# Kernel tuning notes

Hardware: AMD Instinct MI355X
Metric: run time of the kernel (lower is better)

The kernel has to match this reference:

```python
import jax, jax.numpy as jnp
import numpy as np

EPS_ANGLE = 1e-8   # eps in _cos_angle's F.normalize
EPS_NORM = 1e-12   # default F.normalize eps used for the similarity matrix
TOPK = 4
EXTRA_FRAMES = (1, 3, 5, 7)          # teacher-only frames
SHARED_TEACHER = (2, 4, 6)           # shared frames in teacher indexing
SHARED_STUDENT = (1, 2, 3)           # same frames in student indexing
W1 = W2 = W3 = 1.0


def _angle_cosines(ref, shared, sim):
    """Cosines of the 3 RKD angles for every (ref r, shared s, sim k) triplet.
    ref: [B,R,D], shared: [B,S,D], sim: [B,R,K,D]. Returns 3 arrays [B,R,S,K].
    Uses the dot-product expansion (u-v).(w-v) = uw - uv - vw + vv so the
    [B,R,S,K,D] difference tensors are never materialized (same math as the
    chunked torch loop)."""
    rr = jnp.sum(ref * ref, -1)                       # [B,R]
    ss = jnp.sum(shared * shared, -1)                 # [B,S]
    hh = jnp.sum(sim * sim, -1)                       # [B,R,K]
    sr = jnp.einsum('brd,bsd->brs', ref, shared)      # [B,R,S]
    rh = jnp.einsum('brd,brkd->brk', ref, sim)        # [B,R,K]
    sh = jnp.einsum('bsd,brkd->brsk', shared, sim)    # [B,R,S,K]
    rr_ = rr[:, :, None, None]
    ss_ = ss[:, None, :, None]
    hh_ = hh[:, :, None, :]
    sr_ = sr[..., None]
    rh_ = rh[:, :, None, :]
    n_sr = jnp.sqrt(jnp.maximum(ss_ - 2 * sr_ + rr_, 0.0))  # ||shared-ref||
    n_hr = jnp.sqrt(jnp.maximum(hh_ - 2 * rh_ + rr_, 0.0))  # ||sim-ref||
    n_sh = jnp.sqrt(jnp.maximum(ss_ - 2 * sh + hh_, 0.0))   # ||shared-sim||
    cl = lambda n: jnp.maximum(n, EPS_ANGLE)
    a1 = (sh - rh_ - sr_ + rr_) / (cl(n_sr) * cl(n_hr))  # angle at ref
    a2 = (sr_ - sh - rh_ + hh_) / (cl(n_hr) * cl(n_sh))  # angle at sim
    a3 = (rh_ - sr_ - sh + ss_) / (cl(n_sr) * cl(n_sh))  # angle at shared
    return a1, a2, a3


def _l2n(x, eps):
    return x / jnp.maximum(jnp.linalg.norm(x, axis=-1, keepdims=True), eps)


def setup_inputs() -> dict:
    key = jax.random.key(0)
    k1, k2, k3, k4 = jax.random.split(key, 4)
    B, P, D = 4, 1024, 1024
    return {
        'teacher_feats': jax.random.normal(k1, (B, 8, P, D), dtype=jnp.float32),
        'student_feats': jax.random.normal(k2, (B, 4, P, D), dtype=jnp.float32),
        'ref_perm': jax.random.randint(k3, (256,), 0, P),
        'shared_perm': jax.random.randint(k4, (256,), 0, P),
    }


def reference(teacher_feats, student_feats, ref_perm, shared_perm):
    B, St, P, D = teacher_feats.shape
    R = ref_perm.shape[0]
    S = shared_perm.shape[0]
    sg = jax.lax.stop_gradient

    ref_t = sg(teacher_feats[:, 0, ref_perm, :])        # [B,R,D]
    ref_s = student_feats[:, 0, ref_perm, :]            # [B,R,D]

    # teacher-only (extra) frames, concatenated along patch dim -> [B,4P,D]
    extra_t = sg(teacher_feats[:, jnp.array(EXTRA_FRAMES), :, :]).reshape(B, len(EXTRA_FRAMES) * P, D)
    sim = jnp.einsum('brd,bed->bre', _l2n(ref_t, EPS_NORM), _l2n(extra_t, EPS_NORM))
    _, topk_idx = jax.lax.top_k(sim, TOPK)              # [B,R,K]
    sim_high = jax.vmap(lambda e, i: e[i])(extra_t, topk_idx)  # [B,R,K,D]
    sim_high = sg(sim_high)

    s1 = s2 = s3 = jnp.float32(0.0)
    for ti, si in zip(SHARED_TEACHER, SHARED_STUDENT):
        sh_t = sg(teacher_feats[:, ti, shared_perm, :])
        sh_s = student_feats[:, si, shared_perm, :]
        a1t, a2t, a3t = _angle_cosines(ref_t, sh_t, sim_high)
        a1s, a2s, a3s = _angle_cosines(ref_s, sh_s, sim_high)
        s1 = s1 + jnp.sum(jnp.abs(a1s - sg(a1t)))
        s2 = s2 + jnp.sum(jnp.abs(a2s - sg(a2t)))
        s3 = s3 + jnp.sum(jnp.abs(a3s - sg(a3t)))

    total_elements = len(SHARED_TEACHER) * B * R * S * TOPK
    loss = (W1 * s1 + W2 * s2 + W3 * s3) / total_elements
    return loss
```

## Files before the change

kernel.cpp:

```cpp
#include <hip/hip_runtime.h>
#include <float.h>

#define BB 4
#define PP 1024
#define DD 1024
#define RR 256
#define SSZ 256
#define KT 4
#define EE 4096
#define NPAIR 3

typedef float  f32x4  __attribute__((ext_vector_type(4)));
typedef short  short8 __attribute__((ext_vector_type(8)));

#define MFMA16(a,b,c) __builtin_amdgcn_mfma_f32_16x16x32_bf16((a),(b),(c),0,0,0)

#define OFF_NE    ((size_t)0)
#define OFF_RR_T  ((size_t)16384)
#define OFF_RR_S  ((size_t)17408)
#define OFF_HH    ((size_t)18432)
#define OFF_RH_T  ((size_t)22528)
#define OFF_RH_S  ((size_t)26624)
#define OFF_SS_T  ((size_t)30720)
#define OFF_SS_S  ((size_t)33792)
#define OFF_TOPK  ((size_t)36864)
#define OFF_ACC   ((size_t)40960)
#define OFF_CAND  ((size_t)45056)
#define FLOAT_END ((size_t)569344)

#define U_REF_T ((size_t)0)
#define U_REF_S ((size_t)2097152)
#define U_SIMH  ((size_t)4194304)
#define U_SH_T  ((size_t)8388608)
#define U_SH_S  ((size_t)11534336)
#define U_EXT   ((size_t)14680064)

__device__ inline float block_sum256(float v, float* sb) {
  v += __shfl_down(v, 32); v += __shfl_down(v, 16);
  v += __shfl_down(v, 8);  v += __shfl_down(v, 4);
  v += __shfl_down(v, 2);  v += __shfl_down(v, 1);
  int lane = threadIdx.x & 63, wid = threadIdx.x >> 6;
  if (lane == 0) sb[wid] = v;
  __syncthreads();
  float r = 0.f;
  if (threadIdx.x < 4) r = sb[threadIdx.x];
  r += __shfl_down(r, 2); r += __shfl_down(r, 1);
  __syncthreads();
  return r;
}

__device__ inline float dot4(const float4& a, const float4& b) {
  return a.x*b.x + a.y*b.y + a.z*b.z + a.w*b.w;
}

__device__ inline unsigned short bhi(float x) {
  unsigned u = __float_as_uint(x);
  return (unsigned short)((u + 0x7fffu + ((u >> 16) & 1u)) >> 16);
}
__device__ inline ushort4 h4of(float4 f) {
  return make_ushort4(bhi(f.x), bhi(f.y), bhi(f.z), bhi(f.w));
}

__device__ inline size_t wofs(size_t base, int R, int t) {
  int rr = R & 15;
  int ss = ((t >> 1) & 3) ^ ((rr >> 1) & 3);
  return base + (size_t)(R >> 4)*16384 + (size_t)(t >> 3)*512
       + rr*32 + ss*8 + (t & 1)*4;
}

__global__ __launch_bounds__(256) void k_prep(const float* __restrict__ T,
                                              const float* __restrict__ Sf,
                                              const int* __restrict__ ref_perm,
                                              const int* __restrict__ shared_perm,
                                              float* __restrict__ ws) {
  __shared__ float sb[4];
  ushort* uws = (ushort*)(ws + FLOAT_END);
  int blk = blockIdx.x;
  int t = threadIdx.x;
  if (blk < 1024) {
    int b = blk >> 8, r = blk & 255;
    int pos = ref_perm[r];
    const float4* ts = (const float4*)(T  + ((size_t)(b*8 + 0)*PP + pos)*DD);
    const float4* sv = (const float4*)(Sf + ((size_t)(b*4 + 0)*PP + pos)*DD);
    float4 a = ts[t], c = sv[t];
    int R = b*RR + r;
    *(ushort4*)(uws + wofs(U_REF_T, R, t)) = h4of(a);
    *(ushort4*)(uws + wofs(U_REF_S, R, t)) = h4of(c);
    float r1 = block_sum256(dot4(a, a), sb);
    float r2 = block_sum256(dot4(c, c), sb);
    if (t == 0) {
      ws[OFF_RR_T + R] = r1;
      ws[OFF_RR_S + R] = r2;
    }
  } else if (blk < 17408) {
    int i = blk - 1024;
    int b = i >> 12, e = i & 4095;
    int f = 1 + 2*(e >> 10);
    int pos = e & 1023;
    const float4* src = (const float4*)(T + ((size_t)(b*8 + f)*PP + pos)*DD);
    float4 a = src[t];
    *(ushort4*)(uws + wofs(U_EXT, b*EE + e, t)) = h4of(a);
    float tot = block_sum256(dot4(a, a), sb);
    if (t == 0) ws[OFF_NE + (size_t)b*EE + e] = fmaxf(sqrtf(tot), 1e-12f);
  } else {
    int idx = blk - 17408;
    int p = idx / (BB*SSZ);
    int b = (idx / SSZ) % BB;
    int s = idx % SSZ;
    int pos = shared_perm[s];
    int ti = 2*(p + 1), si = p + 1;
    const float4* tr = (const float4*)(T  + ((size_t)(b*8 + ti)*PP + pos)*DD);
    const float4* sr = (const float4*)(Sf + ((size_t)(b*4 + si)*PP + pos)*DD);
    float4 a = tr[t], c = sr[t];
    *(ushort4*)(uws + wofs(U_SH_T, idx, t)) = h4of(a);
    *(ushort4*)(uws + wofs(U_SH_S, idx, t)) = h4of(c);
    float r1 = block_sum256(dot4(a, a), sb);
    float r2 = block_sum256(dot4(c, c), sb);
    if (t == 0) { ws[OFF_SS_T + idx] = r1; ws[OFF_SS_S + idx] = r2; }
  }
}

__global__ __launch_bounds__(256) void k_sim(float* __restrict__ ws) {
  __shared__ float simv[4][16][68];
  const ushort* uws = (const ushort*)(ws + FLOAT_END);
  int d = blockIdx.x;
  int u8 = d & 7, q = d >> 3;
  int b = u8 >> 1, eh = u8 & 1;
  int eb = eh*32 + (q >> 2);
  int rgq = q & 3;
  int tid = threadIdx.x;
  int w = tid >> 6, lane = tid & 63;
  int rg = rgq*4 + w;
  int r0 = rg*16, e0 = eb*64;
  int l15 = lane & 15, lq = (lane >> 4) & 3;
  int laneoff = l15*32 + ((lq ^ ((l15 >> 1) & 3)))*8;

  const ushort* pA = uws + U_REF_T + ((size_t)((b*RR + r0) >> 4))*16384 + laneoff;
  const ushort* pB0 = uws + U_EXT + ((size_t)((b*EE + e0) >> 4) + 0)*16384 + laneoff;
  const ushort* pB1 = uws + U_EXT + ((size_t)((b*EE + e0) >> 4) + 1)*16384 + laneoff;
  const ushort* pB2 = uws + U_EXT + ((size_t)((b*EE + e0) >> 4) + 2)*16384 + laneoff;
  const ushort* pB3 = uws + U_EXT + ((size_t)((b*EE + e0) >> 4) + 3)*16384 + laneoff;

  f32x4 acc[4];
#pragma unroll
  for (int j = 0; j < 4; ++j) acc[j] = (f32x4){0.f, 0.f, 0.f, 0.f};

#pragma unroll 4
  for (int c = 0; c < 32; ++c) {
    int o = c*512;
    short8 ah = *(const short8*)(pA + o);
    short8 b0 = *(const short8*)(pB0 + o);
    short8 b1 = *(const short8*)(pB1 + o);
    short8 b2 = *(const short8*)(pB2 + o);
    short8 b3 = *(const short8*)(pB3 + o);
    acc[0] = MFMA16(ah, b0, acc[0]);
    acc[1] = MFMA16(ah, b1, acc[1]);
    acc[2] = MFMA16(ah, b2, acc[2]);
    acc[3] = MFMA16(ah, b3, acc[3]);
  }

  float invs[4];
#pragma unroll
  for (int j = 0; j < 4; ++j)
    invs[j] = 1.f / ws[OFF_NE + (size_t)b*EE + e0 + j*16 + l15];
#pragma unroll
  for (int j = 0; j < 4; ++j)
#pragma unroll
    for (int q2 = 0; q2 < 4; ++q2)
      simv[w][lq*4 + q2][j*16 + l15] = acc[j][q2] * invs[j];
  if (lane < 16) {
    float v[4] = {-FLT_MAX, -FLT_MAX, -FLT_MAX, -FLT_MAX};
    int ix[4] = {0x7fffffff, 0x7fffffff, 0x7fffffff, 0x7fffffff};
#pragma unroll 1
    for (int e = 0; e < 64; ++e) {
      float f = simv[w][lane][e];
      if (f > v[3]) {
        int eg = e0 + e;
        if (f > v[0])      { v[3]=v[2]; ix[3]=ix[2]; v[2]=v[1]; ix[2]=ix[1]; v[1]=v[0]; ix[1]=ix[0]; v[0]=f; ix[0]=eg; }
        else if (f > v[1]) { v[3]=v[2]; ix[3]=ix[2]; v[2]=v[1]; ix[2]=ix[1]; v[1]=f; ix[1]=eg; }
        else if (f > v[2]) { v[3]=v[2]; ix[3]=ix[2]; v[2]=f; ix[2]=eg; }
        else               { v[3]=f; ix[3]=eg; }
      }
    }
    float2* cand = (float2*)(ws + OFF_CAND);
    size_t base = (((size_t)(b*RR + r0 + lane))*64 + eb)*4;
#pragma unroll
    for (int k = 0; k < 4; ++k)
      cand[base + k] = make_float2(v[k], __int_as_float(ix[k]));
  }
}

__global__ __launch_bounds__(256) void k_select(const float* __restrict__ T,
                                                const float* __restrict__ Sf,
                                                const int* __restrict__ ref_perm,
                                                float* __restrict__ ws) {
  __shared__ float rv[256];
  __shared__ int   ri[256];
  __shared__ int   winIdx;
  __shared__ int   sel[4];
  int br = blockIdx.x;
  int tid = threadIdx.x;
  const float2* cand = (const float2*)(ws + OFF_CAND);
  float2 c0 = cand[(size_t)br*256 + tid];
  float v = c0.x;
  int idx = __float_as_int(c0.y);
  int* outi = (int*)(ws + OFF_TOPK) + (size_t)br*KT;
  for (int k = 0; k < KT; ++k) {
    rv[tid] = v; ri[tid] = idx;
    __syncthreads();
    for (int off = 128; off > 0; off >>= 1) {
      if (tid < off) {
        float v2 = rv[tid+off]; int i2 = ri[tid+off];
        if (v2 > rv[tid] || (v2 == rv[tid] && i2 < ri[tid])) { rv[tid] = v2; ri[tid] = i2; }
      }
      __syncthreads();
    }
    if (tid == 0) { outi[k] = ri[0]; winIdx = ri[0]; sel[k] = ri[0]; }
    __syncthreads();
    if (idx == winIdx) v = -FLT_MAX;
    __syncthreads();
  }

  int b = br >> 8, r = br & 255;
  int g = tid >> 6, lane = tid & 63;
  int e = sel[g];
  int rpos = ref_perm[r];
  const float4* src = (const float4*)(T + ((size_t)(b*8 + 1 + 2*(e >> 10))*PP + (e & 1023))*DD);
  const float4* rt  = (const float4*)(T  + ((size_t)(b*8 + 0)*PP + rpos)*DD);
  const float4* rs  = (const float4*)(Sf + ((size_t)(b*4 + 0)*PP + rpos)*DD);
  ushort* uws = (ushort*)(ws + FLOAT_END);
  int rowi = br*KT + g;
  float hh = 0.f, rht = 0.f, rhs = 0.f;
#pragma unroll
  for (int i = 0; i < 4; ++i) {
    int t4 = lane*4 + i;
    float4 h = src[t4];
    *(ushort4*)(uws + wofs(U_SIMH, rowi, t4)) = h4of(h);
    float4 a = rt[t4], c = rs[t4];
    hh  += dot4(h, h);
    rht += dot4(h, a);
    rhs += dot4(h, c);
  }
  hh  += __shfl_down(hh, 32);  hh  += __shfl_down(hh, 16);
  hh  += __shfl_down(hh, 8);   hh  += __shfl_down(hh, 4);
  hh  += __shfl_down(hh, 2);   hh  += __shfl_down(hh, 1);
  rht += __shfl_down(rht, 32); rht += __shfl_down(rht, 16);
  rht += __shfl_down(rht, 8);  rht += __shfl_down(rht, 4);
  rht += __shfl_down(rht, 2);  rht += __shfl_down(rht, 1);
  rhs += __shfl_down(rhs, 32); rhs += __shfl_down(rhs, 16);
  rhs += __shfl_down(rhs, 8);  rhs += __shfl_down(rhs, 4);
  rhs += __shfl_down(rhs, 2);  rhs += __shfl_down(rhs, 1);
  if (lane == 0) {
    ws[OFF_HH + rowi]   = hh;
    ws[OFF_RH_T + rowi] = rht;
    ws[OFF_RH_S + rowi] = rhs;
  }
}

__global__ __launch_bounds__(192) void k_main(float* __restrict__ ws,
                                              double* __restrict__ acc_out) {
  __shared__ float Ct[3][80][17];
  __shared__ float Cs2[3][80][17];
  __shared__ float sb[3];
  const ushort* uws = (const ushort*)(ws + FLOAT_END);

  int d = blockIdx.x;
  int u8 = d & 7, q = d >> 3;
  int b = u8 >> 1, rhalf = u8 & 1;
  int tid = threadIdx.x;
  int w = tid >> 6, lane = tid & 63;
  int t = q*3 + w;
  int p = t >> 6;
  int rem = t & 63;
  int s32i = rem >> 3, r16q = rem & 7;
  int z = p*4 + b;
  int r16i = rhalf*8 + r16q;
  int r0 = r16i*16, s0 = s32i*32;

  int l15 = lane & 15, lq = (lane >> 4) & 3;
  int laneoff = l15*32 + ((lq ^ ((l15 >> 1) & 3)))*8;

  const ushort* pa0; const ushort* pa1; const ushort* pa2; const ushort* pa3;
  const ushort* prt; const ushort* prs;
  const ushort* pbt0; const ushort* pbt1; const ushort* pbs0; const ushort* pbs1;
  {
    size_t gs = (size_t)((b*RR + r0) >> 2);
    pa0 = uws + U_SIMH + (gs + 0)*16384 + laneoff;
    pa1 = uws + U_SIMH + (gs + 1)*16384 + laneoff;
    pa2 = uws + U_SIMH + (gs + 2)*16384 + laneoff;
    pa3 = uws + U_SIMH + (gs + 3)*16384 + laneoff;
    size_t gr = (size_t)((b*RR + r0) >> 4);
    prt = uws + U_REF_T + gr*16384 + laneoff;
    prs = uws + U_REF_S + gr*16384 + laneoff;
    size_t gh = (size_t)((z*SSZ + s0) >> 4);
    pbt0 = uws + U_SH_T + (gh + 0)*16384 + laneoff;
    pbt1 = uws + U_SH_T + (gh + 1)*16384 + laneoff;
    pbs0 = uws + U_SH_S + (gh + 0)*16384 + laneoff;
    pbs1 = uws + U_SH_S + (gh + 1)*16384 + laneoff;
  }

  f32x4 aT0[2], aT1[2], aT2[2], aT3[2], aRT[2];
  f32x4 aS0[2], aS1[2], aS2[2], aS3[2], aRS[2];
#pragma unroll
  for (int h = 0; h < 2; ++h) {
    aT0[h] = aT1[h] = aT2[h] = aT3[h] = aRT[h] = (f32x4){0.f,0.f,0.f,0.f};
    aS0[h] = aS1[h] = aS2[h] = aS3[h] = aRS[h] = (f32x4){0.f,0.f,0.f,0.f};
  }

#pragma unroll 2
  for (int c = 0; c < 32; ++c) {
    int o = c*512;
    short8 bt0 = *(const short8*)(pbt0 + o);
    short8 bt1 = *(const short8*)(pbt1 + o);
    short8 bs0 = *(const short8*)(pbs0 + o);
    short8 bs1 = *(const short8*)(pbs1 + o);
    short8 a0 = *(const short8*)(pa0 + o);
    short8 a1 = *(const short8*)(pa1 + o);
    short8 a2 = *(const short8*)(pa2 + o);
    short8 a3 = *(const short8*)(pa3 + o);
    short8 rt = *(const short8*)(prt + o);
    short8 rs = *(const short8*)(prs + o);
    aT0[0] = MFMA16(a0, bt0, aT0[0]);  aT0[1] = MFMA16(a0, bt1, aT0[1]);
    aT1[0] = MFMA16(a1, bt0, aT1[0]);  aT1[1] = MFMA16(a1, bt1, aT1[1]);
    aT2[0] = MFMA16(a2, bt0, aT2[0]);  aT2[1] = MFMA16(a2, bt1, aT2[1]);
    aT3[0] = MFMA16(a3, bt0, aT3[0]);  aT3[1] = MFMA16(a3, bt1, aT3[1]);
    aRT[0] = MFMA16(rt, bt0, aRT[0]);  aRT[1] = MFMA16(rt, bt1, aRT[1]);
    aS0[0] = MFMA16(a0, bs0, aS0[0]);  aS0[1] = MFMA16(a0, bs1, aS0[1]);
    aS1[0] = MFMA16(a1, bs0, aS1[0]);  aS1[1] = MFMA16(a1, bs1, aS1[1]);
    aS2[0] = MFMA16(a2, bs0, aS2[0]);  aS2[1] = MFMA16(a2, bs1, aS2[1]);
    aS3[0] = MFMA16(a3, bs0, aS3[0]);  aS3[1] = MFMA16(a3, bs1, aS3[1]);
    aRS[0] = MFMA16(rs, bs0, aRS[0]);  aRS[1] = MFMA16(rs, bs1, aRS[1]);
  }

  int rl = lane >> 2, sg = lane & 3;
  int r = r0 + rl;
  float rrt = ws[OFF_RR_T + b*RR + r];
  float rrs = ws[OFF_RR_S + b*RR + r];
  float hhk[4], rhtk[4], rhsk[4], ihr_t[4], ihr_s[4];
#pragma unroll
  for (int k = 0; k < 4; ++k) {
    int idx = (b*RR + r)*KT + k;
    hhk[k]  = ws[OFF_HH + idx];
    rhtk[k] = ws[OFF_RH_T + idx];
    rhsk[k] = ws[OFF_RH_S + idx];
    float nt = sqrtf(fmaxf(hhk[k] - 2.f*rhtk[k] + rrt, 0.f));
    float ns = sqrtf(fmaxf(hhk[k] - 2.f*rhsk[k] + rrs, 0.f));
    ihr_t[k] = 1.f / fmaxf(nt, 1e-8f);
    ihr_s[k] = 1.f / fmaxf(ns, 1e-8f);
  }

  float local = 0.f;
#pragma unroll
  for (int h = 0; h < 2; ++h) {
#pragma unroll
    for (int q2 = 0; q2 < 4; ++q2) {
      int rg = lq*4 + q2;
      Ct[w][ 0 + rg][l15] = aT0[h][q2];
      Ct[w][16 + rg][l15] = aT1[h][q2];
      Ct[w][32 + rg][l15] = aT2[h][q2];
      Ct[w][48 + rg][l15] = aT3[h][q2];
      Ct[w][64 + rg][l15] = aRT[h][q2];
      Cs2[w][ 0 + rg][l15] = aS0[h][q2];
      Cs2[w][16 + rg][l15] = aS1[h][q2];
      Cs2[w][32 + rg][l15] = aS2[h][q2];
      Cs2[w][48 + rg][l15] = aS3[h][q2];
      Cs2[w][64 + rg][l15] = aRS[h][q2];
    }
#pragma unroll
    for (int j = 0; j < 4; ++j) {
      int sl = sg*4 + j;
      int sidx = z*SSZ + s0 + h*16 + sl;
      float sst = ws[OFF_SS_T + sidx];
      float sss = ws[OFF_SS_S + sidx];
      float srt = Ct[w][64 + rl][sl];
      float srs = Cs2[w][64 + rl][sl];
      float isr_t = 1.f / fmaxf(sqrtf(fmaxf(sst - 2.f*srt + rrt, 0.f)), 1e-8f);
      float isr_s = 1.f / fmaxf(sqrtf(fmaxf(sss - 2.f*srs + rrs, 0.f)), 1e-8f);
#pragma unroll
      for (int k = 0; k < 4; ++k) {
        float sht = Ct[w][rl*4 + k][sl];
        float shs = Cs2[w][rl*4 + k][sl];
        float ish_t = 1.f / fmaxf(sqrtf(fmaxf(sst - 2.f*sht + hhk[k], 0.f)), 1e-8f);
        float ish_s = 1.f / fmaxf(sqrtf(fmaxf(sss - 2.f*shs + hhk[k], 0.f)), 1e-8f);
        float a1t = (sht - rhtk[k] - srt + rrt) * (isr_t * ihr_t[k]);
        float a2t = (srt - sht - rhtk[k] + hhk[k]) * (ihr_t[k] * ish_t);
        float a3t = (rhtk[k] - srt - sht + sst) * (isr_t * ish_t);
        float a1s = (shs - rhsk[k] - srs + rrs) * (isr_s * ihr_s[k]);
        float a2s = (srs - shs - rhsk[k] + hhk[k]) * (ihr_s[k] * ish_s);
        float a3s = (rhsk[k] - srs - shs + sss) * (isr_s * ish_s);
        local += fabsf(a1s - a1t) + fabsf(a2s - a2t) + fabsf(a3s - a3t);
      }
    }
  }

  float v = local;
  v += __shfl_down(v, 32); v += __shfl_down(v, 16);
  v += __shfl_down(v, 8);  v += __shfl_down(v, 4);
  v += __shfl_down(v, 2);  v += __shfl_down(v, 1);
  if (lane == 0) sb[w] = v;
  __syncthreads();
  if (tid == 0) atomicAdd(acc_out, (double)(sb[0] + sb[1] + sb[2]));
}

__global__ void k_final(const double* __restrict__ acc, float* __restrict__ out) {
  out[0] = (float)(acc[0] / 3145728.0);
}

extern "C" void kernel_launch(void* const* d_in, const int* in_sizes, int n_in,
                              void* d_out, int out_size, void* d_ws, size_t ws_size,
                              hipStream_t stream) {
  const float* T  = (const float*)d_in[0];
  const float* Sf = (const float*)d_in[1];
  const int* ref_perm    = (const int*)d_in[2];
  const int* shared_perm = (const int*)d_in[3];
  float* ws = (float*)d_ws;
  double* acc = (double*)(ws + OFF_ACC);

  hipMemsetAsync(acc, 0, sizeof(double), stream);
  k_prep<<<20480, 256, 0, stream>>>(T, Sf, ref_perm, shared_perm, ws);
  k_sim<<<1024, 256, 0, stream>>>(ws);
  k_select<<<BB*RR, 256, 0, stream>>>(T, Sf, ref_perm, ws);
  k_main<<<512, 192, 0, stream>>>(ws, acc);
  k_final<<<1, 1, 0, stream>>>(acc, (float*)d_out);
}
```

Measured before the change: 118.1 us.

## Widen k_main shared tile to 64 columns and fuse final division via last-block counter

Measured after the change: 140.5 us. 1.19x slower.

```diff
diff --git a/kernel.cpp b/kernel.cpp
--- a/kernel.cpp
+++ b/kernel.cpp
@@ -258,7 +258,8 @@
 }
 
 __global__ __launch_bounds__(192) void k_main(float* __restrict__ ws,
-                                              double* __restrict__ acc_out) {
+                                              double* __restrict__ acc_out,
+                                              float* __restrict__ out) {
   __shared__ float Ct[3][80][17];
   __shared__ float Cs2[3][80][17];
   __shared__ float sb[3];
@@ -270,19 +271,19 @@
   int tid = threadIdx.x;
   int w = tid >> 6, lane = tid & 63;
   int t = q*3 + w;
-  int p = t >> 6;
-  int rem = t & 63;
-  int s32i = rem >> 3, r16q = rem & 7;
+  int p = t >> 5;
+  int rem = t & 31;
+  int s64i = rem >> 3, r16q = rem & 7;
   int z = p*4 + b;
   int r16i = rhalf*8 + r16q;
-  int r0 = r16i*16, s0 = s32i*32;
+  int r0 = r16i*16, s0 = s64i*64;
 
   int l15 = lane & 15, lq = (lane >> 4) & 3;
   int laneoff = l15*32 + ((lq ^ ((l15 >> 1) & 3)))*8;
 
   const ushort* pa0; const ushort* pa1; const ushort* pa2; const ushort* pa3;
   const ushort* prt; const ushort* prs;
-  const ushort* pbt0; const ushort* pbt1; const ushort* pbs0; const ushort* pbs1;
+  const ushort* pbt[4]; const ushort* pbs[4];
   {
     size_t gs = (size_t)((b*RR + r0) >> 2);
     pa0 = uws + U_SIMH + (gs + 0)*16384 + laneoff;
@@ -293,43 +294,45 @@
     prt = uws + U_REF_T + gr*16384 + laneoff;
     prs = uws + U_REF_S + gr*16384 + laneoff;
     size_t gh = (size_t)((z*SSZ + s0) >> 4);
-    pbt0 = uws + U_SH_T + (gh + 0)*16384 + laneoff;
-    pbt1 = uws + U_SH_T + (gh + 1)*16384 + laneoff;
-    pbs0 = uws + U_SH_S + (gh + 0)*16384 + laneoff;
-    pbs1 = uws + U_SH_S + (gh + 1)*16384 + laneoff;
-  }
-
-  f32x4 aT0[2], aT1[2], aT2[2], aT3[2], aRT[2];
-  f32x4 aS0[2], aS1[2], aS2[2], aS3[2], aRS[2];
-#pragma unroll
-  for (int h = 0; h < 2; ++h) {
+#pragma unroll
+    for (int j = 0; j < 4; ++j) {
+      pbt[j] = uws + U_SH_T + (gh + j)*16384 + laneoff;
+      pbs[j] = uws + U_SH_S + (gh + j)*16384 + laneoff;
+    }
+  }
+
+  f32x4 aT0[4], aT1[4], aT2[4], aT3[4], aRT[4];
+  f32x4 aS0[4], aS1[4], aS2[4], aS3[4], aRS[4];
+#pragma unroll
+  for (int h = 0; h < 4; ++h) {
     aT0[h] = aT1[h] = aT2[h] = aT3[h] = aRT[h] = (f32x4){0.f,0.f,0.f,0.f};
     aS0[h] = aS1[h] = aS2[h] = aS3[h] = aRS[h] = (f32x4){0.f,0.f,0.f,0.f};
   }
 
-#pragma unroll 2
+#pragma unroll 1
   for (int c = 0; c < 32; ++c) {
     int o = c*512;
-    short8 bt0 = *(const short8*)(pbt0 + o);
-    short8 bt1 = *(const short8*)(pbt1 + o);
-    short8 bs0 = *(const short8*)(pbs0 + o);
-    short8 bs1 = *(const short8*)(pbs1 + o);
     short8 a0 = *(const short8*)(pa0 + o);
     short8 a1 = *(const short8*)(pa1 + o);
     short8 a2 = *(const short8*)(pa2 + o);
     short8 a3 = *(const short8*)(pa3 + o);
     short8 rt = *(const short8*)(prt + o);
     short8 rs = *(const short8*)(prs + o);
-    aT0[0] = MFMA16(a0, bt0, aT0[0]);  aT0[1] = MFMA16(a0, bt1, aT0[1]);
-    aT1[0] = MFMA16(a1, bt0, aT1[0]);  aT1[1] = MFMA16(a1, bt1, aT1[1]);
-    aT2[0] = MFMA16(a2, bt0, aT2[0]);  aT2[1] = MFMA16(a2, bt1, aT2[1]);
-    aT3[0] = MFMA16(a3, bt0, aT3[0]);  aT3[1] = MFMA16(a3, bt1, aT3[1]);
-    aRT[0] = MFMA16(rt, bt0, aRT[0]);  aRT[1] = MFMA16(rt, bt1, aRT[1]);
-    aS0[0] = MFMA16(a0, bs0, aS0[0]);  aS0[1] = MFMA16(a0, bs1, aS0[1]);
-    aS1[0] = MFMA16(a1, bs0, aS1[0]);  aS1[1] = MFMA16(a1, bs1, aS1[1]);
-    aS2[0] = MFMA16(a2, bs0, aS2[0]);  aS2[1] = MFMA16(a2, bs1, aS2[1]);
-    aS3[0] = MFMA16(a3, bs0, aS3[0]);  aS3[1] = MFMA16(a3, bs1, aS3[1]);
-    aRS[0] = MFMA16(rs, bs0, aRS[0]);  aRS[1] = MFMA16(rs, bs1, aRS[1]);
+#pragma unroll
+    for (int h = 0; h < 4; ++h) {
+      short8 bt = *(const short8*)(pbt[h] + o);
+      short8 bs = *(const short8*)(pbs[h] + o);
+      aT0[h] = MFMA16(a0, bt, aT0[h]);
+      aT1[h] = MFMA16(a1, bt, aT1[h]);
+      aT2[h] = MFMA16(a2, bt, aT2[h]);
+      aT3[h] = MFMA16(a3, bt, aT3[h]);
+      aRT[h] = MFMA16(rt, bt, aRT[h]);
+      aS0[h] = MFMA16(a0, bs, aS0[h]);
+      aS1[h] = MFMA16(a1, bs, aS1[h]);
+      aS2[h] = MFMA16(a2, bs, aS2[h]);
+      aS3[h] = MFMA16(a3, bs, aS3[h]);
+      aRS[h] = MFMA16(rs, bs, aRS[h]);
+    }
   }
 
   int rl = lane >> 2, sg = lane & 3;
@@ -351,7 +354,7 @@
 
   float local = 0.f;
 #pragma unroll
-  for (int h = 0; h < 2; ++h) {
+  for (int h = 0; h < 4; ++h) {
 #pragma unroll
     for (int q2 = 0; q2 < 4; ++q2) {
       int rg = lq*4 + q2;
@@ -399,11 +402,17 @@
   v += __shfl_down(v, 2);  v += __shfl_down(v, 1);
   if (lane == 0) sb[w] = v;
   __syncthreads();
-  if (tid == 0) atomicAdd(acc_out, (double)(sb[0] + sb[1] + sb[2]));
-}
-
-__global__ void k_final(const double* __restrict__ acc, float* __restrict__ out) {
-  out[0] = (float)(acc[0] / 3145728.0);
+  if (tid == 0) {
+    atomicAdd(acc_out, (double)(sb[0] + sb[1] + sb[2]));
+    __threadfence();
+    int* cnt = (int*)(acc_out + 1);
+    int prev = atomicAdd(cnt, 1);
+    if (prev == 255) {
+      __threadfence();
+      double total = atomicAdd(acc_out, 0.0);
+      out[0] = (float)(total / 3145728.0);
+    }
+  }
 }
 
 extern "C" void kernel_launch(void* const* d_in, const int* in_sizes, int n_in,
@@ -416,10 +425,9 @@
   float* ws = (float*)d_ws;
   double* acc = (double*)(ws + OFF_ACC);
 
-  hipMemsetAsync(acc, 0, sizeof(double), stream);
+  hipMemsetAsync(acc, 0, 16, stream);
   k_prep<<<20480, 256, 0, stream>>>(T, Sf, ref_perm, shared_perm, ws);
   k_sim<<<1024, 256, 0, stream>>>(ws);
   k_select<<<BB*RR, 256, 0, stream>>>(T, Sf, ref_perm, ws);
-  k_main<<<512, 192, 0, stream>>>(ws, acc);
-  k_final<<<1, 1, 0, stream>>>(acc, (float*)d_out);
-}
+  k_main<<<256, 192, 0, stream>>>(ws, acc, (float*)d_out);
+}
```
